# Kernel optimization log

Hardware: AMD Instinct MI355X
Metric: run time of the kernel (lower is better)

The kernel has to match this reference:

```python
import jax, jax.numpy as jnp
import numpy as np

jax.config.update("jax_enable_x64", True)  # exact int64 fixed-point requantization

QMIN, QMAX = 0, 255  # 8-bit asymmetric activations


def _mul_m0_shift(acc, M0, shift):
    """gemmlowp-style fixed-point rescale: round((acc*M0)>>31) >> shift (rounding)."""
    prod = acc.astype(jnp.int64) * M0.astype(jnp.int64)
    nudge = jnp.where(prod >= 0, jnp.int64(1 << 30), jnp.int64(1 - (1 << 30)))
    hi = (prod + nudge) >> 31  # rounding-doubling high mul
    sh = shift.astype(jnp.int64)
    return (hi + (jnp.int64(1) << (sh - 1))) >> sh  # rounding right shift


def _requant(acc, M0, shift, z_out):
    return jnp.clip(_mul_m0_shift(acc, M0, shift) + z_out, QMIN, QMAX).astype(jnp.int32)


def _qconv(q, w, z_in, M0, shift, z_out, pad):
    # int8-style conv: subtract input zero-point, integer accumulate (exact in fp32
    # since |acc| < 2^24 by construction), then fixed-point requantize.
    xf = (q - z_in).astype(jnp.float32)
    acc = jax.lax.conv_general_dilated(
        xf, w, (1, 1), [(pad, pad), (pad, pad)],
        dimension_numbers=("NCHW", "OIHW", "NCHW"))
    return _requant(jnp.round(acc).astype(jnp.int64), M0, shift, z_out)


def _qbn(q, z_in, w, b, M0, shift, z_out):
    # fused quantized BN: per-channel integer affine + fixed-point requantize
    acc = (q.astype(jnp.int64) - z_in) * w.astype(jnp.int64)[None, :, None, None] \
          + b.astype(jnp.int64)[None, :, None, None]
    return _requant(acc, M0, shift, z_out)


def setup_inputs() -> dict:
    key = jax.random.key(0)
    ks = jax.random.split(key, 10)
    B, Cin, H, W = 32, 256, 56, 56
    width, Cout = 64, 256
    x = jax.random.randint(ks[0], (B, Cin, H, W), 0, 256, dtype=jnp.int32)
    w1 = jax.random.randint(ks[1], (width, Cin, 1, 1), -63, 64).astype(jnp.float32)
    w2 = jax.random.randint(ks[2], (width, width, 3, 3), -63, 64).astype(jnp.float32)
    w3 = jax.random.randint(ks[3], (Cout, width, 1, 1), -63, 64).astype(jnp.float32)
    bn1_w = jax.random.randint(ks[4], (width,), 100, 160).astype(jnp.float32)
    bn1_b = jax.random.randint(ks[5], (width,), -1000, 1000).astype(jnp.float32)
    bn2_w = jax.random.randint(ks[6], (width,), 100, 160).astype(jnp.float32)
    bn2_b = jax.random.randint(ks[7], (width,), -1000, 1000).astype(jnp.float32)
    bn3_w = jax.random.randint(ks[8], (Cout,), 100, 160).astype(jnp.float32)
    bn3_b = jax.random.randint(ks[9], (Cout,), -1000, 1000).astype(jnp.float32)
    conv_zin = jnp.array([128, 128, 128], jnp.int32)
    conv_m0 = jnp.array([1518500250] * 3, jnp.int32)
    conv_shift = jnp.array([9, 9, 9], jnp.int32)
    conv_zout = jnp.array([128, 128, 128], jnp.int32)
    bn_m0 = jnp.array([1073741824] * 3, jnp.int32)
    bn_shift = jnp.array([6, 6, 6], jnp.int32)
    bn_zout = jnp.array([128, 128, 128], jnp.int32)
    add_z = jnp.array([128, 128], jnp.int32)
    add_m0 = jnp.array([1073741824] * 2, jnp.int32)
    add_shift = jnp.array([1, 1], jnp.int32)
    add_zout = jnp.array(128, jnp.int32)
    return dict(x=x, w1=w1, w2=w2, w3=w3,
                bn1_w=bn1_w, bn1_b=bn1_b, bn2_w=bn2_w, bn2_b=bn2_b,
                bn3_w=bn3_w, bn3_b=bn3_b,
                conv_zin=conv_zin, conv_m0=conv_m0, conv_shift=conv_shift,
                conv_zout=conv_zout, bn_m0=bn_m0, bn_shift=bn_shift,
                bn_zout=bn_zout, add_z=add_z, add_m0=add_m0,
                add_shift=add_shift, add_zout=add_zout)


def reference(x, w1, w2, w3, bn1_w, bn1_b, bn2_w, bn2_b, bn3_w, bn3_b,
              conv_zin, conv_m0, conv_shift, conv_zout,
              bn_m0, bn_shift, bn_zout,
              add_z, add_m0, add_shift, add_zout):
    identity = x  # a_bit == target_bit -> rescale_matrix path skipped, conv_x = x
    out = _qconv(x, w1, conv_zin[0], conv_m0[0], conv_shift[0], conv_zout[0], 0)
    out = _qbn(out, conv_zout[0], bn1_w, bn1_b, bn_m0[0], bn_shift[0], bn_zout[0])
    out = _qconv(out, w2, conv_zin[1], conv_m0[1], conv_shift[1], conv_zout[1], 1)
    out = _qbn(out, conv_zout[1], bn2_w, bn2_b, bn_m0[1], bn_shift[1], bn_zout[1])
    out = _qconv(out, w3, conv_zin[2], conv_m0[2], conv_shift[2], conv_zout[2], 0)
    out = _qbn(out, conv_zout[2], bn3_w, bn3_b, bn_m0[2], bn_shift[2], bn_zout[2])
    # QuantizedAdd: rescale both branches to the output scale, add, clamp
    ra = _mul_m0_shift(identity.astype(jnp.int64) - add_z[0], add_m0[0], add_shift[0])
    rb = _mul_m0_shift(out.astype(jnp.int64) - add_z[1], add_m0[1], add_shift[1])
    return jnp.clip(ra + rb + add_zout, QMIN, QMAX).astype(jnp.int32)
```

## Files before the change

### kernel.cpp

```cpp
#include <hip/hip_runtime.h>


typedef int v4i __attribute__((ext_vector_type(4)));

#define BATCH 32
#define CIN 256
#define CMID 64
#define HW 3136
#define W56 56

#define T1_BYTES ((size_t)BATCH * HW * CMID)
#define WP_BYTES ((size_t)68 * 64 * 16)

__device__ __forceinline__ int requant_q(int acc, int M0, int shift, int zout) {
    long long prod = (long long)acc * (long long)M0;
    long long nudge = (prod >= 0) ? (1LL << 30) : (1LL - (1LL << 30));
    long long hi = (prod + nudge) >> 31;
    long long r = (hi + (1LL << (shift - 1))) >> shift;
    int v = (int)r + zout;
    return v < 0 ? 0 : (v > 255 ? 255 : v);
}

__device__ __forceinline__ long long mulshift_ll(long long v, int M0, int shift) {
    long long prod = v * (long long)M0;
    long long nudge = (prod >= 0) ? (1LL << 30) : (1LL - (1LL << 30));
    long long hi = (prod + nudge) >> 31;
    return (hi + (1LL << (shift - 1))) >> shift;
}

__device__ __forceinline__ v4i pack16f(const float* src, int stride) {
    v4i r;
#pragma unroll
    for (int d = 0; d < 4; ++d) {
        unsigned int u = 0;
#pragma unroll
        for (int by = 0; by < 4; ++by) {
            int v = (int)src[(d * 4 + by) * stride];
            u |= ((unsigned int)(v & 255)) << (8 * by);
        }
        r[d] = (int)u;
    }
    return r;
}

__global__ __launch_bounds__(256) void k_prep(
    const float* __restrict__ w1, const float* __restrict__ w2,
    const float* __restrict__ w3, v4i* __restrict__ wp)
{
    int id = blockIdx.x * 256 + threadIdx.x;
    int fid = id >> 6, lane = id & 63;
    if (fid >= 68) return;
    int col = lane & 15, ci0 = (lane >> 4) * 16;
    const float* src;
    int stride;
    if (fid < 16) {
        int wv = fid >> 2, ks = fid & 3;
        src = w1 + (size_t)(wv * 16 + col) * 256 + ks * 64 + ci0;
        stride = 1;
    } else if (fid < 52) {
        int i = fid - 16, wv = i / 9, t = i - wv * 9;
        src = w2 + ((size_t)(wv * 16 + col) * 64 + ci0) * 9 + t;
        stride = 9;
    } else {
        int s = fid - 52;
        src = w3 + (size_t)(s * 16 + col) * 64 + ci0;
        stride = 1;
    }
    wp[fid * 64 + lane] = pack16f(src, stride);
}

__global__ __launch_bounds__(256, 4) void k_conv1(
    const int* __restrict__ x, const v4i* __restrict__ wp1,
    const float* __restrict__ bn_w, const float* __restrict__ bn_b,
    const int* __restrict__ conv_zin, const int* __restrict__ conv_m0,
    const int* __restrict__ conv_shift, const int* __restrict__ conv_zout,
    const int* __restrict__ bn_m0, const int* __restrict__ bn_shift,
    const int* __restrict__ bn_zout, signed char* __restrict__ t1)
{
    __shared__ v4i sm[560];
    const int tid = threadIdx.x, lane = tid & 63, wv = tid >> 6;
    const int col = lane & 15, koff = lane >> 4;
    const int b = blockIdx.y;
    const int hw0 = blockIdx.x * 112;
    const int co0 = wv * 16;

    v4i a[4];
#pragma unroll
    for (int ks = 0; ks < 4; ++ks) a[ks] = wp1[(wv * 4 + ks) * 64 + lane];

    const int cg = tid & 7, q = tid >> 3;
    const bool act = q < 28;
    const int zin = conv_zin[0];
    const int* xbase = x + (size_t)b * CIN * HW + hw0 + 4 * q;

    v4i xa[8], xa2[8];
    if (act) {
#pragma unroll
        for (int j = 0; j < 8; ++j)
            xa[j] = *(const v4i*)(xbase + (size_t)(cg * 8 + j) * HW);
    }

    v4i acc[7];
#pragma unroll
    for (int i = 0; i < 7; ++i) acc[i] = (v4i){0, 0, 0, 0};

    unsigned long long* smu = (unsigned long long*)sm;
#pragma unroll
    for (int ks = 0; ks < 4; ++ks) {
        if (ks) __syncthreads();
        if (act) {
#pragma unroll
            for (int p = 0; p < 4; ++p) {
                unsigned int lo = 0, hi = 0;
#pragma unroll
                for (int j = 0; j < 4; ++j) {
                    lo |= ((unsigned int)((xa[j][p] - zin) & 255)) << (8 * j);
                    hi |= ((unsigned int)((xa[j + 4][p] - zin) & 255)) << (8 * j);
                }
                smu[(q * 4 + p) * 10 + cg] = ((unsigned long long)hi << 32) | lo;
            }
        }
        __syncthreads();
        if (ks < 3 && act) {
#pragma unroll
            for (int j = 0; j < 8; ++j)
                xa2[j] = *(const v4i*)(xbase + (size_t)((ks + 1) * 64 + cg * 8 + j) * HW);
        }
#pragma unroll
        for (int nt = 0; nt < 7; ++nt) {
            v4i bf = sm[(nt * 16 + col) * 5 + koff];
            acc[nt] = __builtin_amdgcn_mfma_i32_16x16x64_i8(a[ks], bf, acc[nt], 0, 0, 0);
        }
        if (ks < 3) {
#pragma unroll
            for (int j = 0; j < 8; ++j) xa[j] = xa2[j];
        }
    }

    const int cm0 = conv_m0[0], csh = conv_shift[0], czo = conv_zout[0];
    const int bm0 = bn_m0[0], bsh = bn_shift[0], bzo = bn_zout[0];
    const int zin2 = conv_zin[1];
    const int rowb = koff * 4;
    int bw[4], bb[4];
#pragma unroll
    for (int r = 0; r < 4; ++r) {
        bw[r] = (int)bn_w[co0 + rowb + r];
        bb[r] = (int)bn_b[co0 + rowb + r];
    }
#pragma unroll
    for (int nt = 0; nt < 7; ++nt) {
        int n = b * HW + hw0 + nt * 16 + col;
        unsigned int pkd = 0;
#pragma unroll
        for (int r = 0; r < 4; ++r) {
            int qv = requant_q(acc[nt][r], cm0, csh, czo);
            int a2 = (qv - czo) * bw[r] + bb[r];
            int q2 = requant_q(a2, bm0, bsh, bzo);
            pkd |= ((unsigned int)((q2 - zin2) & 255)) << (8 * r);
        }
        *(unsigned int*)(t1 + (size_t)n * 64 + co0 + rowb) = pkd;
    }
}

__global__ __launch_bounds__(256) void k_conv2(
    const signed char* __restrict__ t1, const v4i* __restrict__ wp2,
    const float* __restrict__ bn_w, const float* __restrict__ bn_b,
    const int* __restrict__ conv_zin, const int* __restrict__ conv_m0,
    const int* __restrict__ conv_shift, const int* __restrict__ conv_zout,
    const int* __restrict__ bn_m0, const int* __restrict__ bn_shift,
    const int* __restrict__ bn_zout, signed char* __restrict__ t2)
{
    __shared__ v4i sm[1680];
    const int tid = threadIdx.x, lane = tid & 63, wv = tid >> 6;
    const int col = lane & 15, koff = lane >> 4;
    const int b = blockIdx.y;
    const int r0 = blockIdx.x * 4;
    const int co0 = wv * 16;

    v4i a[9];
#pragma unroll
    for (int t = 0; t < 9; ++t) a[t] = wp2[(wv * 9 + t) * 64 + lane];

    const v4i* t1v = (const v4i*)t1;
#pragma unroll
    for (int k = 0; k < 6; ++k) {
        int idx = tid + k * 256;
        if (idx < 1344) {
            int pixl = idx >> 2, part = idx & 3;
            int lrow = pixl / W56, gw = pixl - lrow * W56;
            int grow = r0 - 1 + lrow;
            v4i v = (v4i){0, 0, 0, 0};
            if ((unsigned)grow < 56u)
                v = t1v[((size_t)b * HW + grow * W56 + gw) * 4 + part];
            sm[pixl * 5 + part] = v;
        }
    }
    __syncthreads();

    int orow[14], wc[14];
#pragma unroll
    for (int nt = 0; nt < 14; ++nt) {
        int pix = nt * 16 + col;
        orow[nt] = pix / W56;
        wc[nt] = pix - orow[nt] * W56;
    }

    v4i acc[14];
#pragma unroll
    for (int i = 0; i < 14; ++i) acc[i] = (v4i){0, 0, 0, 0};

#pragma unroll
    for (int kh = 0; kh < 3; ++kh) {
#pragma unroll
        for (int kw = 0; kw < 3; ++kw) {
            v4i af = a[kh * 3 + kw];
#pragma unroll
            for (int nt = 0; nt < 14; ++nt) {
                int sr = orow[nt] + kh;
                int sw = wc[nt] + kw - 1;
                bool valid = (unsigned)sw < 56u;
                v4i bf = sm[(sr * W56 + (valid ? sw : 0)) * 5 + koff];
                if (!valid) { bf[0] = 0; bf[1] = 0; bf[2] = 0; bf[3] = 0; }
                acc[nt] = __builtin_amdgcn_mfma_i32_16x16x64_i8(af, bf, acc[nt], 0, 0, 0);
            }
        }
    }

    const int cm0 = conv_m0[1], csh = conv_shift[1], czo = conv_zout[1];
    const int bm0 = bn_m0[1], bsh = bn_shift[1], bzo = bn_zout[1];
    const int zin3 = conv_zin[2];
    const int rowb = koff * 4;
    int bw[4], bb[4];
#pragma unroll
    for (int r = 0; r < 4; ++r) {
        bw[r] = (int)bn_w[co0 + rowb + r];
        bb[r] = (int)bn_b[co0 + rowb + r];
    }
#pragma unroll
    for (int nt = 0; nt < 14; ++nt) {
        int pix = nt * 16 + col;
        int n = b * HW + r0 * W56 + pix;
        unsigned int pkd = 0;
#pragma unroll
        for (int r = 0; r < 4; ++r) {
            int qv = requant_q(acc[nt][r], cm0, csh, czo);
            int a2 = (qv - czo) * bw[r] + bb[r];
            int q2 = requant_q(a2, bm0, bsh, bzo);
            pkd |= ((unsigned int)((q2 - zin3) & 255)) << (8 * r);
        }
        *(unsigned int*)(t2 + (size_t)n * 64 + co0 + rowb) = pkd;
    }
}

__global__ __launch_bounds__(256, 4) void k_conv3(
    const signed char* __restrict__ t2, const v4i* __restrict__ wp3,
    const float* __restrict__ bn_w, const float* __restrict__ bn_b,
    const int* __restrict__ x,
    const int* __restrict__ conv_m0, const int* __restrict__ conv_shift,
    const int* __restrict__ conv_zout,
    const int* __restrict__ bn_m0, const int* __restrict__ bn_shift,
    const int* __restrict__ bn_zout,
    const int* __restrict__ add_z, const int* __restrict__ add_m0,
    const int* __restrict__ add_shift, const int* __restrict__ add_zout,
    int* __restrict__ out)
{
    __shared__ v4i sm[640];
    const int tid = threadIdx.x, lane = tid & 63, wv = tid >> 6;
    const int col = lane & 15, koff = lane >> 4;
    const int nbase = blockIdx.x * 128;
    const int co0 = blockIdx.y * 64 + wv * 16;
    const int rowb = koff * 4;

    v4i a = wp3[(blockIdx.y * 4 + wv) * 64 + lane];

    int nn[8], pb[8], phw[8];
#pragma unroll
    for (int nt = 0; nt < 8; ++nt) {
        nn[nt] = nbase + nt * 16 + col;
        pb[nt] = nn[nt] / HW;
        phw[nt] = nn[nt] - pb[nt] * HW;
    }
    int xv[8][4];
#pragma unroll
    for (int nt = 0; nt < 8; ++nt)
#pragma unroll
        for (int r = 0; r < 4; ++r)
            xv[nt][r] = x[((size_t)pb[nt] * CIN + co0 + rowb + r) * HW + phw[nt]];

    const v4i* t2v = (const v4i*)t2;
#pragma unroll
    for (int k = 0; k < 2; ++k) {
        int idx = tid + k * 256;
        int pixl = idx >> 2, part = idx & 3;
        sm[pixl * 5 + part] = t2v[(size_t)(nbase + pixl) * 4 + part];
    }
    __syncthreads();

    v4i acc[8];
#pragma unroll
    for (int i = 0; i < 8; ++i) acc[i] = (v4i){0, 0, 0, 0};
#pragma unroll
    for (int nt = 0; nt < 8; ++nt) {
        v4i bf = sm[(nt * 16 + col) * 5 + koff];
        acc[nt] = __builtin_amdgcn_mfma_i32_16x16x64_i8(a, bf, acc[nt], 0, 0, 0);
    }

    const int cm0 = conv_m0[2], csh = conv_shift[2], czo = conv_zout[2];
    const int bm0 = bn_m0[2], bsh = bn_shift[2], bzo = bn_zout[2];
    const int az0 = add_z[0], az1 = add_z[1];
    const int am0 = add_m0[0], am1 = add_m0[1];
    const int ash0 = add_shift[0], ash1 = add_shift[1];
    const int azout = add_zout[0];
    int bw[4], bb[4];
#pragma unroll
    for (int r = 0; r < 4; ++r) {
        bw[r] = (int)bn_w[co0 + rowb + r];
        bb[r] = (int)bn_b[co0 + rowb + r];
    }
#pragma unroll
    for (int nt = 0; nt < 8; ++nt) {
#pragma unroll
        for (int r = 0; r < 4; ++r) {
            int qv = requant_q(acc[nt][r], cm0, csh, czo);
            int a2 = (qv - czo) * bw[r] + bb[r];
            int q2 = requant_q(a2, bm0, bsh, bzo);
            long long ra = mulshift_ll((long long)(xv[nt][r] - az0), am0, ash0);
            long long rb = mulshift_ll((long long)(q2 - az1), am1, ash1);
            int res = (int)(ra + rb) + azout;
            res = res < 0 ? 0 : (res > 255 ? 255 : res);
            out[((size_t)pb[nt] * CIN + co0 + rowb + r) * HW + phw[nt]] = res;
        }
    }
}

extern "C" void kernel_launch(void* const* d_in, const int* in_sizes, int n_in,
                              void* d_out, int out_size, void* d_ws, size_t ws_size,
                              hipStream_t stream) {
    const int* x = (const int*)d_in[0];
    const float* w1 = (const float*)d_in[1];
    const float* w2 = (const float*)d_in[2];
    const float* w3 = (const float*)d_in[3];
    const float* bn1_w = (const float*)d_in[4];
    const float* bn1_b = (const float*)d_in[5];
    const float* bn2_w = (const float*)d_in[6];
    const float* bn2_b = (const float*)d_in[7];
    const float* bn3_w = (const float*)d_in[8];
    const float* bn3_b = (const float*)d_in[9];
    const int* conv_zin = (const int*)d_in[10];
    const int* conv_m0 = (const int*)d_in[11];
    const int* conv_shift = (const int*)d_in[12];
    const int* conv_zout = (const int*)d_in[13];
    const int* bn_m0 = (const int*)d_in[14];
    const int* bn_shift = (const int*)d_in[15];
    const int* bn_zout = (const int*)d_in[16];
    const int* add_z = (const int*)d_in[17];
    const int* add_m0 = (const int*)d_in[18];
    const int* add_shift = (const int*)d_in[19];
    const int* add_zout = (const int*)d_in[20];

    v4i* wp = (v4i*)d_ws;
    signed char* t1 = (signed char*)d_ws + WP_BYTES;
    signed char* t2 = t1 + T1_BYTES;

    const v4i* wp1 = wp;
    const v4i* wp2 = wp + 16 * 64;
    const v4i* wp3 = wp + 52 * 64;

    k_prep<<<dim3(17), dim3(256), 0, stream>>>(w1, w2, w3, wp);
    k_conv1<<<dim3(28, 32), dim3(256), 0, stream>>>(x, wp1, bn1_w, bn1_b,
        conv_zin, conv_m0, conv_shift, conv_zout, bn_m0, bn_shift, bn_zout, t1);
    k_conv2<<<dim3(14, 32), dim3(256), 0, stream>>>(t1, wp2, bn2_w, bn2_b,
        conv_zin, conv_m0, conv_shift, conv_zout, bn_m0, bn_shift, bn_zout, t2);
    k_conv3<<<dim3(784, 4), dim3(256), 0, stream>>>(t2, wp3, bn3_w, bn3_b,
        x, conv_m0, conv_shift, conv_zout, bn_m0, bn_shift, bn_zout,
        add_z, add_m0, add_shift, add_zout, (int*)d_out);
}
```

Measured before the change: 279.4 us.

## Fuse 3x3 conv2 and 1x1 conv3 with residual add into one kernel

```diff
diff --git a/kernel.cpp b/kernel.cpp
--- a/kernel.cpp
+++ b/kernel.cpp
@@ -162,20 +162,28 @@
     }
 }
 
-__global__ __launch_bounds__(256) void k_conv2(
+__global__ __launch_bounds__(256, 3) void k_conv23(
     const signed char* __restrict__ t1, const v4i* __restrict__ wp2,
-    const float* __restrict__ bn_w, const float* __restrict__ bn_b,
+    const v4i* __restrict__ wp3,
+    const float* __restrict__ bn2_w, const float* __restrict__ bn2_b,
+    const float* __restrict__ bn3_w, const float* __restrict__ bn3_b,
+    const int* __restrict__ x,
     const int* __restrict__ conv_zin, const int* __restrict__ conv_m0,
     const int* __restrict__ conv_shift, const int* __restrict__ conv_zout,
     const int* __restrict__ bn_m0, const int* __restrict__ bn_shift,
-    const int* __restrict__ bn_zout, signed char* __restrict__ t2)
+    const int* __restrict__ bn_zout,
+    const int* __restrict__ add_z, const int* __restrict__ add_m0,
+    const int* __restrict__ add_shift, const int* __restrict__ add_zout,
+    int* __restrict__ out)
 {
-    __shared__ v4i sm[1680];
+    __shared__ v4i sm[1120];
+    __shared__ v4i t2s[560];
     const int tid = threadIdx.x, lane = tid & 63, wv = tid >> 6;
     const int col = lane & 15, koff = lane >> 4;
     const int b = blockIdx.y;
-    const int r0 = blockIdx.x * 4;
+    const int r0 = blockIdx.x * 2;
     const int co0 = wv * 16;
+    const int rowb = koff * 4;
 
     v4i a[9];
 #pragma unroll
@@ -183,9 +191,9 @@
 
     const v4i* t1v = (const v4i*)t1;
 #pragma unroll
-    for (int k = 0; k < 6; ++k) {
+    for (int k = 0; k < 4; ++k) {
         int idx = tid + k * 256;
-        if (idx < 1344) {
+        if (idx < 896) {
             int pixl = idx >> 2, part = idx & 3;
             int lrow = pixl / W56, gw = pixl - lrow * W56;
             int grow = r0 - 1 + lrow;
@@ -197,17 +205,17 @@
     }
     __syncthreads();
 
-    int orow[14], wc[14];
-#pragma unroll
-    for (int nt = 0; nt < 14; ++nt) {
+    int orow[7], wc[7];
+#pragma unroll
+    for (int nt = 0; nt < 7; ++nt) {
         int pix = nt * 16 + col;
         orow[nt] = pix / W56;
         wc[nt] = pix - orow[nt] * W56;
     }
 
-    v4i acc[14];
-#pragma unroll
-    for (int i = 0; i < 14; ++i) acc[i] = (v4i){0, 0, 0, 0};
+    v4i acc[7];
+#pragma unroll
+    for (int i = 0; i < 7; ++i) acc[i] = (v4i){0, 0, 0, 0};
 
 #pragma unroll
     for (int kh = 0; kh < 3; ++kh) {
@@ -215,7 +223,7 @@
         for (int kw = 0; kw < 3; ++kw) {
             v4i af = a[kh * 3 + kw];
 #pragma unroll
-            for (int nt = 0; nt < 14; ++nt) {
+            for (int nt = 0; nt < 7; ++nt) {
                 int sr = orow[nt] + kh;
                 int sw = wc[nt] + kw - 1;
                 bool valid = (unsigned)sw < 56u;
@@ -226,84 +234,31 @@
         }
     }
 
-    const int cm0 = conv_m0[1], csh = conv_shift[1], czo = conv_zout[1];
-    const int bm0 = bn_m0[1], bsh = bn_shift[1], bzo = bn_zout[1];
-    const int zin3 = conv_zin[2];
-    const int rowb = koff * 4;
-    int bw[4], bb[4];
-#pragma unroll
-    for (int r = 0; r < 4; ++r) {
-        bw[r] = (int)bn_w[co0 + rowb + r];
-        bb[r] = (int)bn_b[co0 + rowb + r];
-    }
-#pragma unroll
-    for (int nt = 0; nt < 14; ++nt) {
-        int pix = nt * 16 + col;
-        int n = b * HW + r0 * W56 + pix;
-        unsigned int pkd = 0;
+    {
+        const int cm0 = conv_m0[1], csh = conv_shift[1], czo = conv_zout[1];
+        const int bm0 = bn_m0[1], bsh = bn_shift[1], bzo = bn_zout[1];
+        const int zin3 = conv_zin[2];
+        int bw[4], bb[4];
 #pragma unroll
         for (int r = 0; r < 4; ++r) {
-            int qv = requant_q(acc[nt][r], cm0, csh, czo);
-            int a2 = (qv - czo) * bw[r] + bb[r];
-            int q2 = requant_q(a2, bm0, bsh, bzo);
-            pkd |= ((unsigned int)((q2 - zin3) & 255)) << (8 * r);
-        }
-        *(unsigned int*)(t2 + (size_t)n * 64 + co0 + rowb) = pkd;
-    }
-}
-
-__global__ __launch_bounds__(256, 4) void k_conv3(
-    const signed char* __restrict__ t2, const v4i* __restrict__ wp3,
-    const float* __restrict__ bn_w, const float* __restrict__ bn_b,
-    const int* __restrict__ x,
-    const int* __restrict__ conv_m0, const int* __restrict__ conv_shift,
-    const int* __restrict__ conv_zout,
-    const int* __restrict__ bn_m0, const int* __restrict__ bn_shift,
-    const int* __restrict__ bn_zout,
-    const int* __restrict__ add_z, const int* __restrict__ add_m0,
-    const int* __restrict__ add_shift, const int* __restrict__ add_zout,
-    int* __restrict__ out)
-{
-    __shared__ v4i sm[640];
-    const int tid = threadIdx.x, lane = tid & 63, wv = tid >> 6;
-    const int col = lane & 15, koff = lane >> 4;
-    const int nbase = blockIdx.x * 128;
-    const int co0 = blockIdx.y * 64 + wv * 16;
-    const int rowb = koff * 4;
-
-    v4i a = wp3[(blockIdx.y * 4 + wv) * 64 + lane];
-
-    int nn[8], pb[8], phw[8];
-#pragma unroll
-    for (int nt = 0; nt < 8; ++nt) {
-        nn[nt] = nbase + nt * 16 + col;
-        pb[nt] = nn[nt] / HW;
-        phw[nt] = nn[nt] - pb[nt] * HW;
-    }
-    int xv[8][4];
-#pragma unroll
-    for (int nt = 0; nt < 8; ++nt)
-#pragma unroll
-        for (int r = 0; r < 4; ++r)
-            xv[nt][r] = x[((size_t)pb[nt] * CIN + co0 + rowb + r) * HW + phw[nt]];
-
-    const v4i* t2v = (const v4i*)t2;
-#pragma unroll
-    for (int k = 0; k < 2; ++k) {
-        int idx = tid + k * 256;
-        int pixl = idx >> 2, part = idx & 3;
-        sm[pixl * 5 + part] = t2v[(size_t)(nbase + pixl) * 4 + part];
+            bw[r] = (int)bn2_w[co0 + rowb + r];
+            bb[r] = (int)bn2_b[co0 + rowb + r];
+        }
+#pragma unroll
+        for (int nt = 0; nt < 7; ++nt) {
+            int pix = nt * 16 + col;
+            unsigned int pkd = 0;
+#pragma unroll
+            for (int r = 0; r < 4; ++r) {
+                int qv = requant_q(acc[nt][r], cm0, csh, czo);
+                int a2 = (qv - czo) * bw[r] + bb[r];
+                int q2 = requant_q(a2, bm0, bsh, bzo);
+                pkd |= ((unsigned int)((q2 - zin3) & 255)) << (8 * r);
+            }
+            *(unsigned int*)((char*)t2s + (size_t)(pix * 5 + wv) * 16 + koff * 4) = pkd;
+        }
     }
     __syncthreads();
-
-    v4i acc[8];
-#pragma unroll
-    for (int i = 0; i < 8; ++i) acc[i] = (v4i){0, 0, 0, 0};
-#pragma unroll
-    for (int nt = 0; nt < 8; ++nt) {
-        v4i bf = sm[(nt * 16 + col) * 5 + koff];
-        acc[nt] = __builtin_amdgcn_mfma_i32_16x16x64_i8(a, bf, acc[nt], 0, 0, 0);
-    }
 
     const int cm0 = conv_m0[2], csh = conv_shift[2], czo = conv_zout[2];
     const int bm0 = bn_m0[2], bsh = bn_shift[2], bzo = bn_zout[2];
@@ -311,24 +266,51 @@
     const int am0 = add_m0[0], am1 = add_m0[1];
     const int ash0 = add_shift[0], ash1 = add_shift[1];
     const int azout = add_zout[0];
-    int bw[4], bb[4];
-#pragma unroll
-    for (int r = 0; r < 4; ++r) {
-        bw[r] = (int)bn_w[co0 + rowb + r];
-        bb[r] = (int)bn_b[co0 + rowb + r];
-    }
-#pragma unroll
-    for (int nt = 0; nt < 8; ++nt) {
+    const int phw0 = r0 * W56;
+
+#pragma unroll
+    for (int s = 0; s < 4; ++s) {
+        const int c0 = (wv * 4 + s) * 16;
+        v4i a3 = wp3[(wv * 4 + s) * 64 + lane];
+
+        int xv[7][4];
+#pragma unroll
+        for (int nt = 0; nt < 7; ++nt) {
+            int phw = phw0 + nt * 16 + col;
+#pragma unroll
+            for (int r = 0; r < 4; ++r)
+                xv[nt][r] = x[((size_t)b * CIN + c0 + rowb + r) * HW + phw];
+        }
+
+        v4i acc3[7];
+#pragma unroll
+        for (int i = 0; i < 7; ++i) acc3[i] = (v4i){0, 0, 0, 0};
+#pragma unroll
+        for (int nt = 0; nt < 7; ++nt) {
+            v4i bf = t2s[(nt * 16 + col) * 5 + koff];
+            acc3[nt] = __builtin_amdgcn_mfma_i32_16x16x64_i8(a3, bf, acc3[nt], 0, 0, 0);
+        }
+
+        int bw3[4], bb3[4];
 #pragma unroll
         for (int r = 0; r < 4; ++r) {
-            int qv = requant_q(acc[nt][r], cm0, csh, czo);
-            int a2 = (qv - czo) * bw[r] + bb[r];
-            int q2 = requant_q(a2, bm0, bsh, bzo);
-            long long ra = mulshift_ll((long long)(xv[nt][r] - az0), am0, ash0);
-            long long rb = mulshift_ll((long long)(q2 - az1), am1, ash1);
-            int res = (int)(ra + rb) + azout;
-            res = res < 0 ? 0 : (res > 255 ? 255 : res);
-            out[((size_t)pb[nt] * CIN + co0 + rowb + r) * HW + phw[nt]] = res;
+            bw3[r] = (int)bn3_w[c0 + rowb + r];
+            bb3[r] = (int)bn3_b[c0 + rowb + r];
+        }
+#pragma unroll
+        for (int nt = 0; nt < 7; ++nt) {
+            int phw = phw0 + nt * 16 + col;
+#pragma unroll
+            for (int r = 0; r < 4; ++r) {
+                int qv = requant_q(acc3[nt][r], cm0, csh, czo);
+                int a2 = (qv - czo) * bw3[r] + bb3[r];
+                int q2 = requant_q(a2, bm0, bsh, bzo);
+                long long ra = mulshift_ll((long long)(xv[nt][r] - az0), am0, ash0);
+                long long rb = mulshift_ll((long long)(q2 - az1), am1, ash1);
+                int res = (int)(ra + rb) + azout;
+                res = res < 0 ? 0 : (res > 255 ? 255 : res);
+                out[((size_t)b * CIN + c0 + rowb + r) * HW + phw] = res;
+            }
         }
     }
 }
@@ -360,7 +342,6 @@
 
     v4i* wp = (v4i*)d_ws;
     signed char* t1 = (signed char*)d_ws + WP_BYTES;
-    signed char* t2 = t1 + T1_BYTES;
 
     const v4i* wp1 = wp;
     const v4i* wp2 = wp + 16 * 64;
@@ -369,9 +350,8 @@
     k_prep<<<dim3(17), dim3(256), 0, stream>>>(w1, w2, w3, wp);
     k_conv1<<<dim3(28, 32), dim3(256), 0, stream>>>(x, wp1, bn1_w, bn1_b,
         conv_zin, conv_m0, conv_shift, conv_zout, bn_m0, bn_shift, bn_zout, t1);
-    k_conv2<<<dim3(14, 32), dim3(256), 0, stream>>>(t1, wp2, bn2_w, bn2_b,
-        conv_zin, conv_m0, conv_shift, conv_zout, bn_m0, bn_shift, bn_zout, t2);
-    k_conv3<<<dim3(784, 4), dim3(256), 0, stream>>>(t2, wp3, bn3_w, bn3_b,
-        x, conv_m0, conv_shift, conv_zout, bn_m0, bn_shift, bn_zout,
+    k_conv23<<<dim3(28, 32), dim3(256), 0, stream>>>(t1, wp2, wp3,
+        bn2_w, bn2_b, bn3_w, bn3_b, x,
+        conv_zin, conv_m0, conv_shift, conv_zout, bn_m0, bn_shift, bn_zout,
         add_z, add_m0, add_shift, add_zout, (int*)d_out);
 }
```

Result: no change. 282.8 us (+1.2%).
